# Performance work log

Measured on AMD Instinct MI355X. Metric: run time of the kernel, lower is better.

The kernel has to match this reference:

```python
import jax, jax.numpy as jnp
import numpy as np

N = 100000      # num nodes
E = 1600000     # num edges (avg degree 16)
IN = 128        # input_dim
D = 32          # output_dim per head
H = 4           # heads
ALPHA = 0.2     # LeakyReLU slope


def setup_inputs() -> dict:
    key = jax.random.key(0)
    k1, k2, k3, k4, k5 = jax.random.split(key, 5)
    X = jax.random.normal(k1, (N, IN), dtype=jnp.float32)
    # fc weights, xavier-like scale (bias=False in the module)
    W0 = jax.random.normal(k2, (H * D, IN), dtype=jnp.float32) * (1.0 / np.sqrt(IN))
    W1 = jax.random.normal(k3, (H * D, IN), dtype=jnp.float32) * (1.0 / np.sqrt(IN))
    a0 = jax.random.normal(k4, (H, 1, D), dtype=jnp.float32) * (1.0 / np.sqrt(D))
    deg = E // N
    # CSR rows expanded to sorted segment ids: every node has exactly `deg` out-edges
    edge_src = jnp.repeat(jnp.arange(N, dtype=jnp.int32), deg)
    column_index = jax.random.randint(k5, (E,), 0, N, dtype=jnp.int32)
    return {"X": X, "W0": W0, "W1": W1, "a0": a0,
            "edge_src": edge_src, "column_index": column_index}


def _leaky_relu(x):
    return jnp.where(x > 0, x, ALPHA * x)


def reference(X, W0, W1, a0, edge_src, column_index):
    # Linear projections, split per head: [H, N, D]
    X0 = _leaky_relu(X @ W0.T).reshape(N, H, D).transpose(1, 0, 2)
    X1 = _leaky_relu(X @ W1.T).reshape(N, H, D).transpose(1, 0, 2)
    a = a0[:, 0, :]                                    # [H, D]
    # SDDMM: att[h,e] = a[h] . (X0[h,src(e)] + X1[h,dst(e)])
    s0 = jnp.einsum('hnd,hd->hn', X0, a)               # [H, N]
    s1 = jnp.einsum('hnd,hd->hn', X1, a)
    att = s0[:, edge_src] + s1[:, column_index]        # [H, E]
    # per-head global min-max normalization, then exp (module's softmax surrogate)
    mx = jnp.max(att, axis=1, keepdims=True)
    mn = jnp.min(att, axis=1, keepdims=True)
    att = jnp.exp((att - mn) / (mx - mn))
    # sparse row-sum (softmax denominator): [N, H]
    rows_sum = jax.ops.segment_sum(att.T, edge_src, num_segments=N)
    # SpMM: aggregate neighbor features weighted by att -> [N, H, D]
    msg = att.T[:, :, None] * X1[:, column_index, :].transpose(1, 0, 2)  # [E, H, D]
    h_prime = jax.ops.segment_sum(msg, edge_src, num_segments=N)
    return h_prime / rows_sum[:, :, None]
```

## Files before the change

kernel.cpp:

```cpp
#include <hip/hip_runtime.h>
#include <hip/hip_bf16.h>

#define NN 100000
#define EE 1600000
#define ALPHA 0.2f
#define MM_BLOCKS 391

typedef __bf16 bf16_t;
typedef __bf16 bf16x8 __attribute__((ext_vector_type(8)));
typedef __bf16 bf16x4 __attribute__((ext_vector_type(4)));
typedef float fx4 __attribute__((ext_vector_type(4)));


__global__ __launch_bounds__(256) void prep_kernel(
    const float* __restrict__ W0, const float* __restrict__ W1,
    bf16_t* __restrict__ Wb)
{
  const int t = blockIdx.x * 256 + threadIdx.x;
  if (t < 16384)      Wb[t] = (bf16_t)W0[t];
  else if (t < 32768) Wb[t] = (bf16_t)W1[t - 16384];
}

__global__ __launch_bounds__(256) void gemm_kernel(
    const float* __restrict__ X, const bf16_t* __restrict__ Wb,
    const float* __restrict__ a0,
    bf16_t* __restrict__ F1, float* __restrict__ s0g, float* __restrict__ s1g)
{
  const int wv   = threadIdx.x >> 6;
  const int lane = threadIdx.x & 63;
  const int tile = blockIdx.x * 4 + wv;
  if (tile >= (NN / 16)) return;
  const int col  = lane & 15;
  const int quad = lane >> 4;
  const int n0   = tile * 16;

  fx4 a0v[8];
#pragma unroll
  for (int j = 0; j < 8; ++j) a0v[j] = *(const fx4*)(a0 + j * 16 + quad * 4);

  fx4 acc[16];
#pragma unroll
  for (int c = 0; c < 16; ++c) {
    acc[c][0] = 0.f; acc[c][1] = 0.f; acc[c][2] = 0.f; acc[c][3] = 0.f;
  }

  const float* xrow = X + (size_t)(n0 + col) * 128 + quad * 8;
#pragma unroll
  for (int ks = 0; ks < 4; ++ks) {
    fx4 xa = *(const fx4*)(xrow + ks * 32);
    fx4 xb = *(const fx4*)(xrow + ks * 32 + 4);
    bf16x8 xf;
    xf[0] = (bf16_t)xa[0]; xf[1] = (bf16_t)xa[1];
    xf[2] = (bf16_t)xa[2]; xf[3] = (bf16_t)xa[3];
    xf[4] = (bf16_t)xb[0]; xf[5] = (bf16_t)xb[1];
    xf[6] = (bf16_t)xb[2]; xf[7] = (bf16_t)xb[3];
#pragma unroll
    for (int ct = 0; ct < 16; ++ct) {
      bf16x8 wf = *(const bf16x8*)(Wb + (size_t)(ct * 16 + col) * 128 + ks * 32 + quad * 8);
      acc[ct] = __builtin_amdgcn_mfma_f32_16x16x32_bf16(wf, xf, acc[ct], 0, 0, 0);
    }
  }

  const int node = n0 + col;
  float sdot[8];
#pragma unroll
  for (int s = 0; s < 8; ++s) sdot[s] = 0.f;

#pragma unroll
  for (int ct = 0; ct < 16; ++ct) {
#pragma unroll
    for (int r = 0; r < 4; ++r) {
      float v = acc[ct][r];
      v = v > 0.f ? v : ALPHA * v;
      acc[ct][r] = v;
      sdot[ct >> 1] += v * a0v[ct & 7][r];
    }
    if (ct >= 8) {
      bf16x4 p;
      p[0] = (bf16_t)acc[ct][0]; p[1] = (bf16_t)acc[ct][1];
      p[2] = (bf16_t)acc[ct][2]; p[3] = (bf16_t)acc[ct][3];
      *(bf16x4*)(F1 + (size_t)node * 128 + (ct - 8) * 16 + quad * 4) = p;
    }
  }

#pragma unroll
  for (int s = 0; s < 8; ++s) {
    sdot[s] += __shfl_xor(sdot[s], 16);
    sdot[s] += __shfl_xor(sdot[s], 32);
  }
  if (quad == 0) {
    fx4 r0, r1;
    r0[0] = sdot[0]; r0[1] = sdot[1]; r0[2] = sdot[2]; r0[3] = sdot[3];
    r1[0] = sdot[4]; r1[1] = sdot[5]; r1[2] = sdot[6]; r1[3] = sdot[7];
    *(fx4*)(s0g + (size_t)node * 4) = r0;
    *(fx4*)(s1g + (size_t)node * 4) = r1;
  }
}

__global__ __launch_bounds__(256) void minmax1_kernel(
    const int* __restrict__ cidx, const float* __restrict__ s0g,
    const float* __restrict__ s1g, float* __restrict__ partial)
{
  __shared__ float s_red[4][8];
  const int node = blockIdx.x * 256 + threadIdx.x;
  fx4 mx, mn;
#pragma unroll
  for (int h = 0; h < 4; ++h) { mx[h] = -1e30f; mn[h] = 1e30f; }
  if (node < NN) {
    const fx4 s0v = *(const fx4*)(s0g + (size_t)node * 4);
    const int4* ce = (const int4*)(cidx + (size_t)node * 16);
#pragma unroll
    for (int q = 0; q < 4; ++q) {
      const int4 c4 = ce[q];
      const int cc[4] = {c4.x, c4.y, c4.z, c4.w};
#pragma unroll
      for (int j = 0; j < 4; ++j) {
        const fx4 s1v = *(const fx4*)(s1g + (size_t)cc[j] * 4);
#pragma unroll
        for (int h = 0; h < 4; ++h) {
          const float att = s0v[h] + s1v[h];
          mx[h] = fmaxf(mx[h], att);
          mn[h] = fminf(mn[h], att);
        }
      }
    }
  }
#pragma unroll
  for (int off = 1; off < 64; off <<= 1) {
#pragma unroll
    for (int h = 0; h < 4; ++h) {
      mx[h] = fmaxf(mx[h], __shfl_xor(mx[h], off));
      mn[h] = fminf(mn[h], __shfl_xor(mn[h], off));
    }
  }
  const int wv = threadIdx.x >> 6;
  if ((threadIdx.x & 63) == 0) {
#pragma unroll
    for (int h = 0; h < 4; ++h) {
      s_red[wv][h] = mx[h];
      s_red[wv][4 + h] = mn[h];
    }
  }
  __syncthreads();
  if (threadIdx.x < 8) {
    const int s = threadIdx.x;
    float v = s_red[0][s];
    if (s < 4) { v = fmaxf(v, s_red[1][s]); v = fmaxf(v, s_red[2][s]); v = fmaxf(v, s_red[3][s]); }
    else       { v = fminf(v, s_red[1][s]); v = fminf(v, s_red[2][s]); v = fminf(v, s_red[3][s]); }
    partial[blockIdx.x * 8 + s] = v;
  }
}

__global__ __launch_bounds__(256) void minmax2_kernel(
    const float* __restrict__ partial, float* __restrict__ mm)
{
  __shared__ float s_red[4][8];
  fx4 mx, mn;
#pragma unroll
  for (int h = 0; h < 4; ++h) { mx[h] = -1e30f; mn[h] = 1e30f; }
  for (int g = threadIdx.x; g < MM_BLOCKS; g += 256) {
    const fx4 p0 = *(const fx4*)(partial + g * 8);
    const fx4 p1 = *(const fx4*)(partial + g * 8 + 4);
#pragma unroll
    for (int h = 0; h < 4; ++h) {
      mx[h] = fmaxf(mx[h], p0[h]);
      mn[h] = fminf(mn[h], p1[h]);
    }
  }
#pragma unroll
  for (int off = 1; off < 64; off <<= 1) {
#pragma unroll
    for (int h = 0; h < 4; ++h) {
      mx[h] = fmaxf(mx[h], __shfl_xor(mx[h], off));
      mn[h] = fminf(mn[h], __shfl_xor(mn[h], off));
    }
  }
  const int wv = threadIdx.x >> 6;
  if ((threadIdx.x & 63) == 0) {
#pragma unroll
    for (int h = 0; h < 4; ++h) {
      s_red[wv][h] = mx[h];
      s_red[wv][4 + h] = mn[h];
    }
  }
  __syncthreads();
  if (threadIdx.x < 8) {
    const int s = threadIdx.x;
    float v = s_red[0][s];
    if (s < 4) { v = fmaxf(v, s_red[1][s]); v = fmaxf(v, s_red[2][s]); v = fmaxf(v, s_red[3][s]); }
    else       { v = fminf(v, s_red[1][s]); v = fminf(v, s_red[2][s]); v = fminf(v, s_red[3][s]); }
    mm[s] = v;
  }
}

__global__ __launch_bounds__(256) void aggregate_kernel(
    const int* __restrict__ cidx, const float* __restrict__ s0g,
    const float* __restrict__ s1g, const bf16_t* __restrict__ F1,
    const float* __restrict__ mm, float* __restrict__ out)
{
  const int t = blockIdx.x * 256 + threadIdx.x;
  const int node = t >> 5;
  if (node >= NN) return;
  const int sub = t & 31;
  const int h = sub >> 3;
  const float mxv = mm[h];
  const float mnv = mm[4 + h];
  const float scale = 1.f / (mxv - mnv);
  const float s0v = s0g[node * 4 + h];
  float a0_ = 0.f, a1_ = 0.f, a2_ = 0.f, a3_ = 0.f, wsum = 0.f;
  const int* ce = cidx + node * 16;
#pragma unroll
  for (int e = 0; e < 16; ++e) {
    const int c = ce[e];
    const float att = s0v + s1g[c * 4 + h];
    const float w = __expf((att - mnv) * scale);
    bf16x4 f = *(const bf16x4*)(F1 + (size_t)c * 128 + sub * 4);
    a0_ += w * (float)f[0];
    a1_ += w * (float)f[1];
    a2_ += w * (float)f[2];
    a3_ += w * (float)f[3];
    wsum += w;
  }
  const float inv = 1.f / wsum;
  fx4 res;
  res[0] = a0_ * inv; res[1] = a1_ * inv; res[2] = a2_ * inv; res[3] = a3_ * inv;
  *(fx4*)(out + (size_t)node * 128 + sub * 4) = res;
}

extern "C" void kernel_launch(void* const* d_in, const int* in_sizes, int n_in,
                              void* d_out, int out_size, void* d_ws, size_t ws_size,
                              hipStream_t stream)
{
  const float* X   = (const float*)d_in[0];
  const float* W0  = (const float*)d_in[1];
  const float* W1  = (const float*)d_in[2];
  const float* a0  = (const float*)d_in[3];
  const int* cidx  = (const int*)d_in[5];
  char* ws = (char*)d_ws;
  bf16_t*   Wb      = (bf16_t*)(ws);
  bf16_t*   F1      = (bf16_t*)(ws + 65536);
  float*    s0g     = (float*)(ws + 25665536);
  float*    s1g     = (float*)(ws + 27265536);
  float*    mm      = (float*)(ws + 28865536);
  float*    partial = (float*)(ws + 28865600);
  float*    out     = (float*)d_out;

  prep_kernel<<<128, 256, 0, stream>>>(W0, W1, Wb);
  gemm_kernel<<<1563, 256, 0, stream>>>(X, Wb, a0, F1, s0g, s1g);
  minmax1_kernel<<<MM_BLOCKS, 256, 0, stream>>>(cidx, s0g, s1g, partial);
  minmax2_kernel<<<1, 256, 0, stream>>>(partial, mm);
  aggregate_kernel<<<12500, 256, 0, stream>>>(cidx, s0g, s1g, F1, mm, out);
}
```

Before: 242.3 us.

## Split GEMM tiles across wave pairs, parallelize minmax per edge-quad, widen aggregate loads

```diff
diff --git a/kernel.cpp b/kernel.cpp
--- a/kernel.cpp
+++ b/kernel.cpp
@@ -4,7 +4,7 @@
 #define NN 100000
 #define EE 1600000
 #define ALPHA 0.2f
-#define MM_BLOCKS 391
+#define MM_BLOCKS 1563
 
 typedef __bf16 bf16_t;
 typedef __bf16 bf16x8 __attribute__((ext_vector_type(8)));
@@ -28,19 +28,17 @@
 {
   const int wv   = threadIdx.x >> 6;
   const int lane = threadIdx.x & 63;
-  const int tile = blockIdx.x * 4 + wv;
+  const int tile = blockIdx.x * 2 + (wv >> 1);
   if (tile >= (NN / 16)) return;
+  const int half = wv & 1;
   const int col  = lane & 15;
   const int quad = lane >> 4;
   const int n0   = tile * 16;
-
-  fx4 a0v[8];
-#pragma unroll
-  for (int j = 0; j < 8; ++j) a0v[j] = *(const fx4*)(a0 + j * 16 + quad * 4);
-
-  fx4 acc[16];
-#pragma unroll
-  for (int c = 0; c < 16; ++c) {
+  const int ctb  = half * 8;
+
+  fx4 acc[8];
+#pragma unroll
+  for (int c = 0; c < 8; ++c) {
     acc[c][0] = 0.f; acc[c][1] = 0.f; acc[c][2] = 0.f; acc[c][3] = 0.f;
   }
 
@@ -55,45 +53,43 @@
     xf[4] = (bf16_t)xb[0]; xf[5] = (bf16_t)xb[1];
     xf[6] = (bf16_t)xb[2]; xf[7] = (bf16_t)xb[3];
 #pragma unroll
-    for (int ct = 0; ct < 16; ++ct) {
-      bf16x8 wf = *(const bf16x8*)(Wb + (size_t)(ct * 16 + col) * 128 + ks * 32 + quad * 8);
-      acc[ct] = __builtin_amdgcn_mfma_f32_16x16x32_bf16(wf, xf, acc[ct], 0, 0, 0);
+    for (int c = 0; c < 8; ++c) {
+      bf16x8 wf = *(const bf16x8*)(Wb + (size_t)((ctb + c) * 16 + col) * 128 + ks * 32 + quad * 8);
+      acc[c] = __builtin_amdgcn_mfma_f32_16x16x32_bf16(wf, xf, acc[c], 0, 0, 0);
     }
   }
 
   const int node = n0 + col;
-  float sdot[8];
-#pragma unroll
-  for (int s = 0; s < 8; ++s) sdot[s] = 0.f;
-
-#pragma unroll
-  for (int ct = 0; ct < 16; ++ct) {
+  float sdot[4] = {0.f, 0.f, 0.f, 0.f};
+
+#pragma unroll
+  for (int c = 0; c < 8; ++c) {
+    const fx4 av = *(const fx4*)(a0 + c * 16 + quad * 4);
 #pragma unroll
     for (int r = 0; r < 4; ++r) {
-      float v = acc[ct][r];
+      float v = acc[c][r];
       v = v > 0.f ? v : ALPHA * v;
-      acc[ct][r] = v;
-      sdot[ct >> 1] += v * a0v[ct & 7][r];
-    }
-    if (ct >= 8) {
+      acc[c][r] = v;
+      sdot[c >> 1] += v * av[r];
+    }
+    if (half) {
       bf16x4 p;
-      p[0] = (bf16_t)acc[ct][0]; p[1] = (bf16_t)acc[ct][1];
-      p[2] = (bf16_t)acc[ct][2]; p[3] = (bf16_t)acc[ct][3];
-      *(bf16x4*)(F1 + (size_t)node * 128 + (ct - 8) * 16 + quad * 4) = p;
-    }
-  }
-
-#pragma unroll
-  for (int s = 0; s < 8; ++s) {
+      p[0] = (bf16_t)acc[c][0]; p[1] = (bf16_t)acc[c][1];
+      p[2] = (bf16_t)acc[c][2]; p[3] = (bf16_t)acc[c][3];
+      *(bf16x4*)(F1 + (size_t)node * 128 + c * 16 + quad * 4) = p;
+    }
+  }
+
+#pragma unroll
+  for (int s = 0; s < 4; ++s) {
     sdot[s] += __shfl_xor(sdot[s], 16);
     sdot[s] += __shfl_xor(sdot[s], 32);
   }
   if (quad == 0) {
-    fx4 r0, r1;
-    r0[0] = sdot[0]; r0[1] = sdot[1]; r0[2] = sdot[2]; r0[3] = sdot[3];
-    r1[0] = sdot[4]; r1[1] = sdot[5]; r1[2] = sdot[6]; r1[3] = sdot[7];
-    *(fx4*)(s0g + (size_t)node * 4) = r0;
-    *(fx4*)(s1g + (size_t)node * 4) = r1;
+    fx4 rr;
+    rr[0] = sdot[0]; rr[1] = sdot[1]; rr[2] = sdot[2]; rr[3] = sdot[3];
+    if (half) *(fx4*)(s1g + (size_t)node * 4) = rr;
+    else      *(fx4*)(s0g + (size_t)node * 4) = rr;
   }
 }
 
@@ -102,26 +98,23 @@
     const float* __restrict__ s1g, float* __restrict__ partial)
 {
   __shared__ float s_red[4][8];
-  const int node = blockIdx.x * 256 + threadIdx.x;
+  const int t = blockIdx.x * 256 + threadIdx.x;
   fx4 mx, mn;
 #pragma unroll
   for (int h = 0; h < 4; ++h) { mx[h] = -1e30f; mn[h] = 1e30f; }
-  if (node < NN) {
+  if (t < EE / 4) {
+    const int node = t >> 2;
     const fx4 s0v = *(const fx4*)(s0g + (size_t)node * 4);
-    const int4* ce = (const int4*)(cidx + (size_t)node * 16);
-#pragma unroll
-    for (int q = 0; q < 4; ++q) {
-      const int4 c4 = ce[q];
-      const int cc[4] = {c4.x, c4.y, c4.z, c4.w};
-#pragma unroll
-      for (int j = 0; j < 4; ++j) {
-        const fx4 s1v = *(const fx4*)(s1g + (size_t)cc[j] * 4);
-#pragma unroll
-        for (int h = 0; h < 4; ++h) {
-          const float att = s0v[h] + s1v[h];
-          mx[h] = fmaxf(mx[h], att);
-          mn[h] = fminf(mn[h], att);
-        }
+    const int4 c4 = ((const int4*)cidx)[t];
+    const int cc[4] = {c4.x, c4.y, c4.z, c4.w};
+#pragma unroll
+    for (int j = 0; j < 4; ++j) {
+      const fx4 s1v = *(const fx4*)(s1g + (size_t)cc[j] * 4);
+#pragma unroll
+      for (int h = 0; h < 4; ++h) {
+        const float att = s0v[h] + s1v[h];
+        mx[h] = fmaxf(mx[h], att);
+        mn[h] = fminf(mn[h], att);
       }
     }
   }
@@ -199,32 +192,34 @@
     const float* __restrict__ mm, float* __restrict__ out)
 {
   const int t = blockIdx.x * 256 + threadIdx.x;
-  const int node = t >> 5;
+  const int node = t >> 4;
   if (node >= NN) return;
-  const int sub = t & 31;
-  const int h = sub >> 3;
+  const int sub = t & 15;
+  const int h = sub >> 2;
   const float mxv = mm[h];
   const float mnv = mm[4 + h];
   const float scale = 1.f / (mxv - mnv);
   const float s0v = s0g[node * 4 + h];
-  float a0_ = 0.f, a1_ = 0.f, a2_ = 0.f, a3_ = 0.f, wsum = 0.f;
+  float a_[8] = {0.f, 0.f, 0.f, 0.f, 0.f, 0.f, 0.f, 0.f};
+  float wsum = 0.f;
   const int* ce = cidx + node * 16;
 #pragma unroll
   for (int e = 0; e < 16; ++e) {
     const int c = ce[e];
     const float att = s0v + s1g[c * 4 + h];
     const float w = __expf((att - mnv) * scale);
-    bf16x4 f = *(const bf16x4*)(F1 + (size_t)c * 128 + sub * 4);
-    a0_ += w * (float)f[0];
-    a1_ += w * (float)f[1];
-    a2_ += w * (float)f[2];
-    a3_ += w * (float)f[3];
+    bf16x8 f = *(const bf16x8*)(F1 + (size_t)c * 128 + sub * 8);
+#pragma unroll
+    for (int j = 0; j < 8; ++j) a_[j] += w * (float)f[j];
     wsum += w;
   }
   const float inv = 1.f / wsum;
-  fx4 res;
-  res[0] = a0_ * inv; res[1] = a1_ * inv; res[2] = a2_ * inv; res[3] = a3_ * inv;
-  *(fx4*)(out + (size_t)node * 128 + sub * 4) = res;
+  fx4 r0, r1;
+#pragma unroll
+  for (int j = 0; j < 4; ++j) { r0[j] = a_[j] * inv; r1[j] = a_[4 + j] * inv; }
+  float* op = out + (size_t)node * 128 + sub * 8;
+  *(fx4*)op = r0;
+  *(fx4*)(op + 4) = r1;
 }
 
 extern "C" void kernel_launch(void* const* d_in, const int* in_sizes, int n_in,
@@ -246,8 +241,8 @@
   float*    out     = (float*)d_out;
 
   prep_kernel<<<128, 256, 0, stream>>>(W0, W1, Wb);
-  gemm_kernel<<<1563, 256, 0, stream>>>(X, Wb, a0, F1, s0g, s1g);
+  gemm_kernel<<<3125, 256, 0, stream>>>(X, Wb, a0, F1, s0g, s1g);
   minmax1_kernel<<<MM_BLOCKS, 256, 0, stream>>>(cidx, s0g, s1g, partial);
   minmax2_kernel<<<1, 256, 0, stream>>>(partial, mm);
-  aggregate_kernel<<<12500, 256, 0, stream>>>(cidx, s0g, s1g, F1, mm, out);
-}
+  aggregate_kernel<<<6250, 256, 0, stream>>>(cidx, s0g, s1g, F1, mm, out);
+}
```

After: 248.1 us. +2.4%, slower.

## Stage weights in LDS, spread minmax over edges, widen aggregate loads

Applied to the files above, without the earlier changes.

```diff
diff --git a/kernel.cpp b/kernel.cpp
--- a/kernel.cpp
+++ b/kernel.cpp
@@ -4,7 +4,7 @@
 #define NN 100000
 #define EE 1600000
 #define ALPHA 0.2f
-#define MM_BLOCKS 391
+#define MM_BLOCKS 1563
 
 typedef __bf16 bf16_t;
 typedef __bf16 bf16x8 __attribute__((ext_vector_type(8)));
@@ -26,17 +26,26 @@
     const float* __restrict__ a0,
     bf16_t* __restrict__ F1, float* __restrict__ s0g, float* __restrict__ s1g)
 {
-  const int wv   = threadIdx.x >> 6;
-  const int lane = threadIdx.x & 63;
+  __shared__ uint4 lw[4096];
+  const int tid  = threadIdx.x;
+  const int wv   = tid >> 6;
+  const int lane = tid & 63;
+  const int col  = lane & 15;
+  const int quad = lane >> 4;
+
+  const uint4* wb4 = (const uint4*)Wb;
+#pragma unroll
+  for (int i = 0; i < 16; ++i) {
+    const int task = i * 256 + tid;
+    const int sct = task >> 8, sks = (task >> 6) & 3, sl = task & 63;
+    lw[task] = wb4[(sct * 16 + (sl & 15)) * 16 + sks * 4 + (sl >> 4)];
+  }
+  __syncthreads();
+
   const int tile = blockIdx.x * 4 + wv;
   if (tile >= (NN / 16)) return;
-  const int col  = lane & 15;
-  const int quad = lane >> 4;
   const int n0   = tile * 16;
-
-  fx4 a0v[8];
-#pragma unroll
-  for (int j = 0; j < 8; ++j) a0v[j] = *(const fx4*)(a0 + j * 16 + quad * 4);
+  const int node = n0 + col;
 
   fx4 acc[16];
 #pragma unroll
@@ -44,7 +53,7 @@
     acc[c][0] = 0.f; acc[c][1] = 0.f; acc[c][2] = 0.f; acc[c][3] = 0.f;
   }
 
-  const float* xrow = X + (size_t)(n0 + col) * 128 + quad * 8;
+  const float* xrow = X + (size_t)node * 128 + quad * 8;
 #pragma unroll
   for (int ks = 0; ks < 4; ++ks) {
     fx4 xa = *(const fx4*)(xrow + ks * 32);
@@ -56,24 +65,25 @@
     xf[6] = (bf16_t)xb[2]; xf[7] = (bf16_t)xb[3];
 #pragma unroll
     for (int ct = 0; ct < 16; ++ct) {
-      bf16x8 wf = *(const bf16x8*)(Wb + (size_t)(ct * 16 + col) * 128 + ks * 32 + quad * 8);
+      const uint4 w4 = lw[(ct * 4 + ks) * 64 + lane];
+      const bf16x8 wf = __builtin_bit_cast(bf16x8, w4);
       acc[ct] = __builtin_amdgcn_mfma_f32_16x16x32_bf16(wf, xf, acc[ct], 0, 0, 0);
     }
   }
 
-  const int node = n0 + col;
   float sdot[8];
 #pragma unroll
   for (int s = 0; s < 8; ++s) sdot[s] = 0.f;
 
 #pragma unroll
   for (int ct = 0; ct < 16; ++ct) {
+    const fx4 av = *(const fx4*)(a0 + (ct & 7) * 16 + quad * 4);
 #pragma unroll
     for (int r = 0; r < 4; ++r) {
       float v = acc[ct][r];
       v = v > 0.f ? v : ALPHA * v;
       acc[ct][r] = v;
-      sdot[ct >> 1] += v * a0v[ct & 7][r];
+      sdot[ct >> 1] += v * av[r];
     }
     if (ct >= 8) {
       bf16x4 p;
@@ -102,26 +112,23 @@
     const float* __restrict__ s1g, float* __restrict__ partial)
 {
   __shared__ float s_red[4][8];
-  const int node = blockIdx.x * 256 + threadIdx.x;
+  const int t = blockIdx.x * 256 + threadIdx.x;
   fx4 mx, mn;
 #pragma unroll
   for (int h = 0; h < 4; ++h) { mx[h] = -1e30f; mn[h] = 1e30f; }
-  if (node < NN) {
+  if (t < EE / 4) {
+    const int node = t >> 2;
     const fx4 s0v = *(const fx4*)(s0g + (size_t)node * 4);
-    const int4* ce = (const int4*)(cidx + (size_t)node * 16);
-#pragma unroll
-    for (int q = 0; q < 4; ++q) {
-      const int4 c4 = ce[q];
-      const int cc[4] = {c4.x, c4.y, c4.z, c4.w};
-#pragma unroll
-      for (int j = 0; j < 4; ++j) {
-        const fx4 s1v = *(const fx4*)(s1g + (size_t)cc[j] * 4);
-#pragma unroll
-        for (int h = 0; h < 4; ++h) {
-          const float att = s0v[h] + s1v[h];
-          mx[h] = fmaxf(mx[h], att);
-          mn[h] = fminf(mn[h], att);
-        }
+    const int4 c4 = ((const int4*)cidx)[t];
+    const int cc[4] = {c4.x, c4.y, c4.z, c4.w};
+#pragma unroll
+    for (int j = 0; j < 4; ++j) {
+      const fx4 s1v = *(const fx4*)(s1g + (size_t)cc[j] * 4);
+#pragma unroll
+      for (int h = 0; h < 4; ++h) {
+        const float att = s0v[h] + s1v[h];
+        mx[h] = fmaxf(mx[h], att);
+        mn[h] = fminf(mn[h], att);
       }
     }
   }
@@ -199,32 +206,39 @@
     const float* __restrict__ mm, float* __restrict__ out)
 {
   const int t = blockIdx.x * 256 + threadIdx.x;
-  const int node = t >> 5;
+  const int node = t >> 4;
   if (node >= NN) return;
-  const int sub = t & 31;
-  const int h = sub >> 3;
+  const int sub = t & 15;
+  const int h = sub >> 2;
   const float mxv = mm[h];
   const float mnv = mm[4 + h];
   const float scale = 1.f / (mxv - mnv);
   const float s0v = s0g[node * 4 + h];
-  float a0_ = 0.f, a1_ = 0.f, a2_ = 0.f, a3_ = 0.f, wsum = 0.f;
-  const int* ce = cidx + node * 16;
-#pragma unroll
-  for (int e = 0; e < 16; ++e) {
-    const int c = ce[e];
-    const float att = s0v + s1g[c * 4 + h];
-    const float w = __expf((att - mnv) * scale);
-    bf16x4 f = *(const bf16x4*)(F1 + (size_t)c * 128 + sub * 4);
-    a0_ += w * (float)f[0];
-    a1_ += w * (float)f[1];
-    a2_ += w * (float)f[2];
-    a3_ += w * (float)f[3];
-    wsum += w;
+  float a_[8] = {0.f, 0.f, 0.f, 0.f, 0.f, 0.f, 0.f, 0.f};
+  float wsum = 0.f;
+  const int4* ce4 = (const int4*)(cidx + (size_t)node * 16);
+#pragma unroll
+  for (int q = 0; q < 4; ++q) {
+    const int4 c4 = ce4[q];
+    const int cc[4] = {c4.x, c4.y, c4.z, c4.w};
+#pragma unroll
+    for (int j = 0; j < 4; ++j) {
+      const int c = cc[j];
+      const float att = s0v + s1g[c * 4 + h];
+      const float w = __expf((att - mnv) * scale);
+      bf16x8 f = *(const bf16x8*)(F1 + (size_t)c * 128 + sub * 8);
+#pragma unroll
+      for (int k = 0; k < 8; ++k) a_[k] += w * (float)f[k];
+      wsum += w;
+    }
   }
   const float inv = 1.f / wsum;
-  fx4 res;
-  res[0] = a0_ * inv; res[1] = a1_ * inv; res[2] = a2_ * inv; res[3] = a3_ * inv;
-  *(fx4*)(out + (size_t)node * 128 + sub * 4) = res;
+  fx4 r0, r1;
+#pragma unroll
+  for (int j = 0; j < 4; ++j) { r0[j] = a_[j] * inv; r1[j] = a_[4 + j] * inv; }
+  float* op = out + (size_t)node * 128 + sub * 8;
+  *(fx4*)op = r0;
+  *(fx4*)(op + 4) = r1;
 }
 
 extern "C" void kernel_launch(void* const* d_in, const int* in_sizes, int n_in,
@@ -249,5 +263,5 @@
   gemm_kernel<<<1563, 256, 0, stream>>>(X, Wb, a0, F1, s0g, s1g);
   minmax1_kernel<<<MM_BLOCKS, 256, 0, stream>>>(cidx, s0g, s1g, partial);
   minmax2_kernel<<<1, 256, 0, stream>>>(partial, mm);
-  aggregate_kernel<<<12500, 256, 0, stream>>>(cidx, s0g, s1g, F1, mm, out);
-}
+  aggregate_kernel<<<6250, 256, 0, stream>>>(cidx, s0g, s1g, F1, mm, out);
+}
```

New measurement: 215.2 us. -11.2%, faster.
